# Kernel tuning notes

Measured on AMD Instinct MI355X. Metric: run time of the kernel, lower is better.

Reference implementation:

```python
import jax, jax.numpy as jnp
import numpy as np

# Mamba-2 dims (from wrapper: d_model=hidden_size=2048, d_state=64, d_conv=4, expand=2, headdim=64)
D_MODEL = 2048
EXPAND = 2
HEADDIM = 64
D_STATE = 64
D_CONV = 4
D_INNER = EXPAND * D_MODEL            # 4096
NHEADS = D_INNER // HEADDIM           # 64
NGROUPS = 1                           # mamba_ssm default
CONV_DIM = D_INNER + 2 * NGROUPS * D_STATE          # 4224
D_IN_PROJ = 2 * D_INNER + 2 * NGROUPS * D_STATE + NHEADS  # 8384
BATCH = 1
SEQLEN = 1024
RMS_EPS = 1e-5


def setup_inputs() -> dict:
    key = jax.random.key(0)
    ks = jax.random.split(key, 8)
    x = jax.random.normal(ks[0], (BATCH, SEQLEN, D_MODEL), jnp.float32)
    W_in = jax.random.normal(ks[1], (D_IN_PROJ, D_MODEL), jnp.float32) * 0.02
    conv_w = jax.random.normal(ks[2], (CONV_DIM, D_CONV), jnp.float32) * 0.2
    conv_b = jnp.zeros((CONV_DIM,), jnp.float32)
    # dt_bias so that softplus(dt_raw + dt_bias) lands in a realistic dt range ~[1e-3, 5e-2]
    dt_bias = jax.random.uniform(ks[3], (NHEADS,), jnp.float32, -6.0, -3.0)
    # A = -exp(A_log), A_log init like mamba_ssm: A ~ Uniform(1, 16)
    A_log = jnp.log(1.0 + 15.0 * jax.random.uniform(ks[4], (NHEADS,), jnp.float32))
    D = jnp.ones((NHEADS,), jnp.float32)
    norm_w = jnp.ones((D_INNER,), jnp.float32)
    W_out = jax.random.normal(ks[5], (D_MODEL, D_INNER), jnp.float32) * 0.02
    return {"x": x, "W_in": W_in, "conv_w": conv_w, "conv_b": conv_b,
            "dt_bias": dt_bias, "A_log": A_log, "D": D, "norm_w": norm_w, "W_out": W_out}


def reference(x, W_in, conv_w, conv_b, dt_bias, A_log, D, norm_w, W_out):
    B, T, _ = x.shape
    # input projection -> [z | xBC | dt]
    zxbcdt = jnp.einsum('btd,pd->btp', x, W_in)
    z = zxbcdt[..., :D_INNER]                                  # [B,T,D_INNER] gate
    xBC = zxbcdt[..., D_INNER:D_INNER + CONV_DIM]              # [B,T,CONV_DIM]
    dt = jax.nn.softplus(zxbcdt[..., D_INNER + CONV_DIM:] + dt_bias)  # [B,T,H]
    # causal depthwise conv1d (kernel D_CONV) + SiLU
    xp = jnp.pad(xBC, ((0, 0), (D_CONV - 1, 0), (0, 0)))
    conv = conv_b + sum(xp[:, k:k + T, :] * conv_w[:, k] for k in range(D_CONV))
    xBC = jax.nn.silu(conv)
    xh = xBC[..., :D_INNER].reshape(B, T, NHEADS, HEADDIM)     # [B,T,H,P]
    Bm = xBC[..., D_INNER:D_INNER + D_STATE]                   # [B,T,N] (ngroups=1)
    Cm = xBC[..., D_INNER + D_STATE:]                          # [B,T,N]
    A = -jnp.exp(A_log)                                        # [H], negative
    dA = jnp.exp(dt * A)                                       # [B,T,H] decay per step

    def step(h, inp):
        # h: [B,H,P,N]
        dA_t, dt_t, B_t, x_t, C_t = inp
        h = h * dA_t[:, :, None, None] + jnp.einsum('bh,bn,bhp->bhpn', dt_t, B_t, x_t)
        y_t = jnp.einsum('bhpn,bn->bhp', h, C_t)
        return h, y_t

    h0 = jnp.zeros((B, NHEADS, HEADDIM, D_STATE), x.dtype)
    xs = (dA.transpose(1, 0, 2), dt.transpose(1, 0, 2), Bm.transpose(1, 0, 2),
          xh.transpose(1, 0, 2, 3), Cm.transpose(1, 0, 2))
    _, ys = jax.lax.scan(step, h0, xs)                         # ys: [T,B,H,P]
    y = ys.transpose(1, 0, 2, 3) + D[None, None, :, None] * xh  # skip term D*x
    y = y.reshape(B, T, D_INNER)
    # gated RMSNorm (norm_before_gate=False): norm(y * silu(z)) * weight
    y = y * jax.nn.silu(z)
    y = y * jax.lax.rsqrt(jnp.mean(y * y, axis=-1, keepdims=True) + RMS_EPS) * norm_w
    return jnp.einsum('bti,di->btd', y, W_out)
```

## Files before the change

### kernel.cpp

```cpp
#include <hip/hip_runtime.h>
#include <hip/hip_bf16.h>
#include <stdint.h>

#define SEQLEN   1024
#define DMODEL   2048
#define DINNER   4096
#define NHEADS   64
#define HEADDIM  64
#define DSTATE   64
#define CONVDIM  4224
#define DINPROJ  8384
#define RMS_EPS  1e-5f
#define CPAD     68

typedef __attribute__((ext_vector_type(8))) __bf16 bf16x8;
typedef __attribute__((ext_vector_type(4))) float f32x4;

__device__ __forceinline__ ushort f2bf(float f) {
    uint32_t u = __float_as_uint(f);
    u += 0x7FFFu + ((u >> 16) & 1u);
    return (ushort)(u >> 16);
}

__device__ __forceinline__ float silu(float a) { return a / (1.f + __expf(-a)); }

__device__ __forceinline__ void gload_lds16(const void* g, void* l) {
    __builtin_amdgcn_global_load_lds(
        (const __attribute__((address_space(1))) void*)g,
        (__attribute__((address_space(3))) void*)l, 16, 0, 0);
}

__global__ __launch_bounds__(256) void cvt3_kernel(
    const float* __restrict__ a, ushort* __restrict__ oa, int na4,
    const float* __restrict__ b, ushort* __restrict__ ob, int nb4,
    const float* __restrict__ c, ushort* __restrict__ oc, int nc4)
{
    int i = blockIdx.x * 256 + threadIdx.x;
    const float* src; ushort* dst;
    if (i < na4) { src = a; dst = oa; }
    else if (i < na4 + nb4) { i -= na4; src = b; dst = ob; }
    else { i -= na4 + nb4; if (i >= nc4) return; src = c; dst = oc; }
    float4 v = ((const float4*)src)[i];
    ushort4 o;
    o.x = f2bf(v.x); o.y = f2bf(v.y); o.z = f2bf(v.z); o.w = f2bf(v.w);
    ((ushort4*)dst)[i] = o;
}

__global__ __launch_bounds__(256, 2) void gemm4_bf16_nt(
    const __bf16* __restrict__ A, const __bf16* __restrict__ B,
    float* __restrict__ C, int M, int N, int K,
    int ntx, int nty, int nk, int ksteps, int swz)
{
    __shared__ __align__(16) __bf16 As[2][128 * 64];
    __shared__ __align__(16) __bf16 Bs[2][128 * 64];
    const int tid  = threadIdx.x;
    const int lane = tid & 63;
    const int wave = tid >> 6;
    const int wr = wave >> 1, wc = wave & 1;
    int id = blockIdx.x;
    if (swz) { int q = (ntx * nty * nk) >> 3; id = (id & 7) * q + (id >> 3); }
    const int kz  = id / (ntx * nty);
    const int rem = id % (ntx * nty);
    const int tx = rem / nty, ty = rem % nty;
    const int row0 = ty * 128, col0 = tx * 128;
    const int lr = lane & 15, lq = lane >> 4;
    const int rA = lane >> 3, jl = lane & 7;
    const int k0 = kz * ksteps * 64;

    const __bf16* srcA[4];
    const __bf16* srcB[4];
    int dstAB[4];
    #pragma unroll
    for (int e = 0; e < 4; ++e) {
        int r0 = (wave * 4 + e) * 8;
        int r  = r0 + rA;
        int jg = jl ^ (r & 7);
        srcA[e] = A + (size_t)(row0 + r) * K + k0 + jg * 8;
        int gb = col0 + r; if (gb > N - 1) gb = N - 1;
        srcB[e] = B + (size_t)gb * K + k0 + jg * 8;
        dstAB[e] = r0 * 64;
    }

    f32x4 acc[4][4] = {};
    const int nt = ksteps;

#define STAGE(BUF)                                                            \
    _Pragma("unroll")                                                         \
    for (int e = 0; e < 4; ++e) {                                             \
        gload_lds16(srcA[e], &As[BUF][dstAB[e]]);                             \
        gload_lds16(srcB[e], &Bs[BUF][dstAB[e]]);                             \
        srcA[e] += 64; srcB[e] += 64;                                         \
    }

#define COMPUTE(BUF)                                                          \
    _Pragma("unroll")                                                         \
    for (int kk = 0; kk < 2; ++kk) {                                          \
        const int kg = kk * 4 + lq;                                           \
        bf16x8 af[4], bfr[4];                                                 \
        _Pragma("unroll")                                                     \
        for (int m = 0; m < 4; ++m) {                                         \
            int r = wr * 64 + m * 16 + lr;                                    \
            af[m] = *(const bf16x8*)(&As[BUF][r * 64 + ((kg ^ (r & 7)) * 8)]);\
        }                                                                     \
        _Pragma("unroll")                                                     \
        for (int n = 0; n < 4; ++n) {                                         \
            int r = wc * 64 + n * 16 + lr;                                    \
            bfr[n] = *(const bf16x8*)(&Bs[BUF][r * 64 + ((kg ^ (r & 7)) * 8)]);\
        }                                                                     \
        __builtin_amdgcn_s_setprio(1);                                        \
        _Pragma("unroll")                                                     \
        for (int m = 0; m < 4; ++m)                                           \
            _Pragma("unroll")                                                 \
            for (int n = 0; n < 4; ++n)                                       \
                acc[m][n] = __builtin_amdgcn_mfma_f32_16x16x32_bf16(af[m], bfr[n], acc[m][n], 0, 0, 0); \
        __builtin_amdgcn_s_setprio(0);                                        \
    }

    STAGE(0);
    asm volatile("s_waitcnt vmcnt(0)" ::: "memory");
    __builtin_amdgcn_s_barrier();
    asm volatile("" ::: "memory");

    for (int t = 0; t < nt; t += 2) {
        STAGE(1);
        COMPUTE(0);
        asm volatile("s_waitcnt vmcnt(0)" ::: "memory");
        __builtin_amdgcn_s_barrier();
        asm volatile("" ::: "memory");
        if (t + 2 < nt) { STAGE(0); }
        COMPUTE(1);
        asm volatile("s_waitcnt vmcnt(0)" ::: "memory");
        __builtin_amdgcn_s_barrier();
        asm volatile("" ::: "memory");
    }
#undef STAGE
#undef COMPUTE

    float* Co = C + (size_t)kz * M * N;
    #pragma unroll
    for (int m = 0; m < 4; ++m)
        #pragma unroll
        for (int n = 0; n < 4; ++n) {
            int col = col0 + wc * 64 + n * 16 + lr;
            if (col < N) {
                #pragma unroll
                for (int j = 0; j < 4; ++j) {
                    int row = row0 + wr * 64 + m * 16 + lq * 4 + j;
                    Co[(size_t)row * N + col] = acc[m][n][j];
                }
            }
        }
}

__global__ __launch_bounds__(256) void reduce4_scale_kernel(
    const float* __restrict__ p, const float* __restrict__ ssbuf,
    float* __restrict__ out, int n4)
{
    int i = blockIdx.x * 256 + threadIdx.x;
    if (i < n4) {
        int t = i >> 9;
        float sc = rsqrtf(ssbuf[t] * (1.f / DINNER) + RMS_EPS);
        float4 a = ((const float4*)p)[i];
        float4 b = ((const float4*)p)[i + n4];
        float4 c = ((const float4*)p)[i + 2 * (size_t)n4];
        float4 d = ((const float4*)p)[i + 3 * (size_t)n4];
        float4 o = {(a.x + b.x + c.x + d.x) * sc, (a.y + b.y + c.y + d.y) * sc,
                    (a.z + b.z + c.z + d.z) * sc, (a.w + b.w + c.w + d.w) * sc};
        ((float4*)out)[i] = o;
    }
}

__global__ __launch_bounds__(256) void chunk_intra_kernel(
    const float* __restrict__ zx, const float* __restrict__ conv_w,
    const float* __restrict__ conv_b, const float* __restrict__ dt_bias,
    const float* __restrict__ A_log,
    float* __restrict__ x_scan, float* __restrict__ Cb,
    float* __restrict__ yintra, float* __restrict__ Tc, float* __restrict__ Ssum)
{
    const int head  = blockIdx.x >> 4;
    const int chunk = blockIdx.x & 15;
    const int t0 = chunk * 64;
    const int tid = threadIdx.x;
    const int ty = tid >> 4, tx = tid & 15;
    const int lane = tid & 63, wv = tid >> 6;

    __shared__ __align__(16) float Xs [64][CPAD];
    __shared__ __align__(16) float BsT[64][CPAD];
    __shared__ __align__(16) float CsT[64][CPAD];
    __shared__ __align__(16) float GsT[64][CPAD];
    __shared__ float Sc[64], dts[64], ws[64];

    {
        const int c0 = head * 64 + tx * 4;
        float4 w0 = *(const float4*)&conv_w[(c0 + 0) * 4];
        float4 w1 = *(const float4*)&conv_w[(c0 + 1) * 4];
        float4 w2 = *(const float4*)&conv_w[(c0 + 2) * 4];
        float4 w3 = *(const float4*)&conv_w[(c0 + 3) * 4];
        float4 bv = *(const float4*)&conv_b[c0];
        #pragma unroll
        for (int pass = 0; pass < 4; ++pass) {
            int s = pass * 16 + ty;
            int gt = t0 + s;
            float4 r0 = {0,0,0,0}, r1 = {0,0,0,0}, r2 = {0,0,0,0}, r3;
            const float* base = zx + (size_t)gt * DINPROJ + DINNER + c0;
            if (gt >= 3) r0 = *(const float4*)(base - 3 * DINPROJ);
            if (gt >= 2) r1 = *(const float4*)(base - 2 * DINPROJ);
            if (gt >= 1) r2 = *(const float4*)(base - 1 * DINPROJ);
            r3 = *(const float4*)base;
            float4 o;
            o.x = silu(bv.x + r0.x*w0.x + r1.x*w0.y + r2.x*w0.z + r3.x*w0.w);
            o.y = silu(bv.y + r0.y*w1.x + r1.y*w1.y + r2.y*w1.z + r3.y*w1.w);
            o.z = silu(bv.z + r0.z*w2.x + r1.z*w2.y + r2.z*w2.z + r3.z*w2.w);
            o.w = silu(bv.w + r0.w*w3.x + r1.w*w3.y + r2.w*w3.z + r3.w*w3.w);
            *(float4*)&Xs[s][tx * 4] = o;
            *(float4*)&x_scan[(size_t)gt * DINNER + head * 64 + tx * 4] = o;
        }
    }

    #pragma unroll
    for (int k = 0; k < 4; ++k) {
        int n0 = wv * 16 + k * 4;
        int gt = t0 + lane;
        {
            float4 w0 = *(const float4*)&conv_w[(4096 + n0 + 0) * 4];
            float4 w1 = *(const float4*)&conv_w[(4096 + n0 + 1) * 4];
            float4 w2 = *(const float4*)&conv_w[(4096 + n0 + 2) * 4];
            float4 w3 = *(const float4*)&conv_w[(4096 + n0 + 3) * 4];
            float4 bv = *(const float4*)&conv_b[4096 + n0];
            float4 r0 = {0,0,0,0}, r1 = {0,0,0,0}, r2 = {0,0,0,0}, r3;
            const float* base = zx + (size_t)gt * DINPROJ + 8192 + n0;
            if (gt >= 3) r0 = *(const float4*)(base - 3 * DINPROJ);
            if (gt >= 2) r1 = *(const float4*)(base - 2 * DINPROJ);
            if (gt >= 1) r2 = *(const float4*)(base - 1 * DINPROJ);
            r3 = *(const float4*)base;
            BsT[n0+0][lane] = silu(bv.x + r0.x*w0.x + r1.x*w0.y + r2.x*w0.z + r3.x*w0.w);
            BsT[n0+1][lane] = silu(bv.y + r0.y*w1.x + r1.y*w1.y + r2.y*w1.z + r3.y*w1.w);
            BsT[n0+2][lane] = silu(bv.z + r0.z*w2.x + r1.z*w2.y + r2.z*w2.z + r3.z*w2.w);
            BsT[n0+3][lane] = silu(bv.w + r0.w*w3.x + r1.w*w3.y + r2.w*w3.z + r3.w*w3.w);
        }
        {
            float4 w0 = *(const float4*)&conv_w[(4160 + n0 + 0) * 4];
            float4 w1 = *(const float4*)&conv_w[(4160 + n0 + 1) * 4];
            float4 w2 = *(const float4*)&conv_w[(4160 + n0 + 2) * 4];
            float4 w3 = *(const float4*)&conv_w[(4160 + n0 + 3) * 4];
            float4 bv = *(const float4*)&conv_b[4160 + n0];
            float4 r0 = {0,0,0,0}, r1 = {0,0,0,0}, r2 = {0,0,0,0}, r3;
            const float* base = zx + (size_t)gt * DINPROJ + 8256 + n0;
            if (gt >= 3) r0 = *(const float4*)(base - 3 * DINPROJ);
            if (gt >= 2) r1 = *(const float4*)(base - 2 * DINPROJ);
            if (gt >= 1) r2 = *(const float4*)(base - 1 * DINPROJ);
            r3 = *(const float4*)base;
            float4 cv;
            cv.x = silu(bv.x + r0.x*w0.x + r1.x*w0.y + r2.x*w0.z + r3.x*w0.w);
            cv.y = silu(bv.y + r0.y*w1.x + r1.y*w1.y + r2.y*w1.z + r3.y*w1.w);
            cv.z = silu(bv.z + r0.z*w2.x + r1.z*w2.y + r2.z*w2.z + r3.z*w2.w);
            cv.w = silu(bv.w + r0.w*w3.x + r1.w*w3.y + r2.w*w3.z + r3.w*w3.w);
            CsT[n0+0][lane] = cv.x; CsT[n0+1][lane] = cv.y;
            CsT[n0+2][lane] = cv.z; CsT[n0+3][lane] = cv.w;
            if (head == 0) *(float4*)&Cb[(size_t)gt * 64 + n0] = cv;
        }
    }

    if (wv == 1) {
        float raw = zx[(size_t)(t0 + lane) * DINPROJ + 8320 + head] + dt_bias[head];
        float dt  = (raw > 20.f) ? raw : log1pf(__expf(raw));
        dts[lane] = dt;
        float v = dt * (-__expf(A_log[head]));
        #pragma unroll
        for (int off = 1; off < 64; off <<= 1) {
            float u = __shfl_up(v, off, 64);
            if (lane >= off) v += u;
        }
        Sc[lane] = v;
        Ssum[(t0 + lane) * 64 + head] = v;
    }
    __syncthreads();
    if (tid < 64) ws[tid] = dts[tid] * __expf(Sc[63] - Sc[tid]);

    float gacc[4][4] = {};
    for (int n = 0; n < 64; ++n) {
        float4 ci = *(const float4*)&CsT[n][ty * 4];
        float4 bs = *(const float4*)&BsT[n][tx * 4];
        gacc[0][0] += ci.x*bs.x; gacc[0][1] += ci.x*bs.y; gacc[0][2] += ci.x*bs.z; gacc[0][3] += ci.x*bs.w;
        gacc[1][0] += ci.y*bs.x; gacc[1][1] += ci.y*bs.y; gacc[1][2] += ci.y*bs.z; gacc[1][3] += ci.y*bs.w;
        gacc[2][0] += ci.z*bs.x; gacc[2][1] += ci.z*bs.y; gacc[2][2] += ci.z*bs.z; gacc[2][3] += ci.z*bs.w;
        gacc[3][0] += ci.w*bs.x; gacc[3][1] += ci.w*bs.y; gacc[3][2] += ci.w*bs.z; gacc[3][3] += ci.w*bs.w;
    }
    {
        float Si[4];
        #pragma unroll
        for (int di = 0; di < 4; ++di) Si[di] = Sc[ty * 4 + di];
        #pragma unroll
        for (int ds = 0; ds < 4; ++ds) {
            int s = tx * 4 + ds;
            float dw = dts[s], Ss_ = Sc[s];
            float4 g;
            g.x = (s <= ty*4+0) ? gacc[0][ds] * dw * __expf(Si[0] - Ss_) : 0.f;
            g.y = (s <= ty*4+1) ? gacc[1][ds] * dw * __expf(Si[1] - Ss_) : 0.f;
            g.z = (s <= ty*4+2) ? gacc[2][ds] * dw * __expf(Si[2] - Ss_) : 0.f;
            g.w = (s <= ty*4+3) ? gacc[3][ds] * dw * __expf(Si[3] - Ss_) : 0.f;
            *(float4*)&GsT[s][ty * 4] = g;
        }
    }
    __syncthreads();
    {
        int nn = wv * 16 + (lane >> 2);
        int s0 = (lane & 3) * 16;
        #pragma unroll
        for (int k = 0; k < 4; ++k) {
            float4 b = *(const float4*)&BsT[nn][s0 + k * 4];
            CsT[s0 + k*4 + 0][nn] = b.x;
            CsT[s0 + k*4 + 1][nn] = b.y;
            CsT[s0 + k*4 + 2][nn] = b.z;
            CsT[s0 + k*4 + 3][nn] = b.w;
        }
    }
    __syncthreads();

    float yacc[4][4] = {};
    float tacc[4][4] = {};
    for (int s = 0; s < 64; ++s) {
        float4 g  = *(const float4*)&GsT[s][ty * 4];
        float4 xp = *(const float4*)&Xs[s][tx * 4];
        float4 xq = *(const float4*)&Xs[s][ty * 4];
        float4 bn = *(const float4*)&CsT[s][tx * 4];
        float w = ws[s];
        yacc[0][0] += g.x*xp.x; yacc[0][1] += g.x*xp.y; yacc[0][2] += g.x*xp.z; yacc[0][3] += g.x*xp.w;
        yacc[1][0] += g.y*xp.x; yacc[1][1] += g.y*xp.y; yacc[1][2] += g.y*xp.z; yacc[1][3] += g.y*xp.w;
        yacc[2][0] += g.z*xp.x; yacc[2][1] += g.z*xp.y; yacc[2][2] += g.z*xp.z; yacc[2][3] += g.z*xp.w;
        yacc[3][0] += g.w*xp.x; yacc[3][1] += g.w*xp.y; yacc[3][2] += g.w*xp.z; yacc[3][3] += g.w*xp.w;
        float wx0 = xq.x * w, wx1 = xq.y * w, wx2 = xq.z * w, wx3 = xq.w * w;
        tacc[0][0] += wx0*bn.x; tacc[0][1] += wx0*bn.y; tacc[0][2] += wx0*bn.z; tacc[0][3] += wx0*bn.w;
        tacc[1][0] += wx1*bn.x; tacc[1][1] += wx1*bn.y; tacc[1][2] += wx1*bn.z; tacc[1][3] += wx1*bn.w;
        tacc[2][0] += wx2*bn.x; tacc[2][1] += wx2*bn.y; tacc[2][2] += wx2*bn.z; tacc[2][3] += wx2*bn.w;
        tacc[3][0] += wx3*bn.x; tacc[3][1] += wx3*bn.y; tacc[3][2] += wx3*bn.z; tacc[3][3] += wx3*bn.w;
    }
    #pragma unroll
    for (int di = 0; di < 4; ++di) {
        float4 yv = {yacc[di][0], yacc[di][1], yacc[di][2], yacc[di][3]};
        *(float4*)&yintra[(size_t)(t0 + ty*4 + di) * DINNER + head * 64 + tx * 4] = yv;
    }
    float* tcb = Tc + (size_t)(head * 16 + chunk) * 4096;
    #pragma unroll
    for (int dq = 0; dq < 4; ++dq) {
        float4 tv = {tacc[dq][0], tacc[dq][1], tacc[dq][2], tacc[dq][3]};
        *(float4*)&tcb[(ty*4 + dq) * 64 + tx * 4] = tv;
    }
}

__global__ __launch_bounds__(256) void chunk_state_kernel(
    float* __restrict__ Tc, const float* __restrict__ Ssum)
{
    const int head = blockIdx.x;
    const int tid = threadIdx.x;
    float h[16] = {};
    float* base = Tc + (size_t)head * 16 * 4096 + tid * 16;
    for (int c = 0; c < 16; ++c) {
        float Q = __expf(Ssum[(c * 64 + 63) * 64 + head]);
        float4* p = (float4*)(base + (size_t)c * 4096);
        #pragma unroll
        for (int v = 0; v < 4; ++v) {
            float4 t = p[v];
            float4 hold = {h[v*4], h[v*4+1], h[v*4+2], h[v*4+3]};
            h[v*4+0] = h[v*4+0] * Q + t.x;
            h[v*4+1] = h[v*4+1] * Q + t.y;
            h[v*4+2] = h[v*4+2] * Q + t.z;
            h[v*4+3] = h[v*4+3] * Q + t.w;
            p[v] = hold;
        }
    }
}

__global__ __launch_bounds__(256) void inter_combine_kernel(
    const float* __restrict__ Hpre, const float* __restrict__ Cb,
    const float* __restrict__ Ssum, const float* __restrict__ yintra,
    const float* __restrict__ x_scan, const float* __restrict__ zx,
    const float* __restrict__ Dv, const float* __restrict__ norm_w,
    ushort* __restrict__ ybf, float* __restrict__ ssbuf)
{
    const int head  = blockIdx.x >> 4;
    const int chunk = blockIdx.x & 15;
    const int t0 = chunk * 64;
    const int tid = threadIdx.x;
    const int ty = tid >> 4, tx = tid & 15;
    const int lane = tid & 63, wv = tid >> 6;

    __shared__ __align__(16) float HsT[64][CPAD];
    __shared__ __align__(16) float CsT[64][CPAD];
    __shared__ float Se[64];

    const float* hb = Hpre + (size_t)(head * 16 + chunk) * 4096;
    #pragma unroll
    for (int k = 0; k < 4; ++k) {
        int n0 = wv * 16 + k * 4;
        float4 h = *(const float4*)&hb[lane * 64 + n0];
        float4 c = *(const float4*)&Cb[(t0 + lane) * 64 + n0];
        HsT[n0][lane] = h.x; HsT[n0+1][lane] = h.y; HsT[n0+2][lane] = h.z; HsT[n0+3][lane] = h.w;
        CsT[n0][lane] = c.x; CsT[n0+1][lane] = c.y; CsT[n0+2][lane] = c.z; CsT[n0+3][lane] = c.w;
    }
    if (tid < 64) Se[tid] = __expf(Ssum[(t0 + tid) * 64 + head]);
    __syncthreads();

    float acc[4][4] = {};
    for (int n = 0; n < 64; ++n) {
        float4 ci = *(const float4*)&CsT[n][ty * 4];
        float4 hp = *(const float4*)&HsT[n][tx * 4];
        acc[0][0] += ci.x*hp.x; acc[0][1] += ci.x*hp.y; acc[0][2] += ci.x*hp.z; acc[0][3] += ci.x*hp.w;
        acc[1][0] += ci.y*hp.x; acc[1][1] += ci.y*hp.y; acc[1][2] += ci.y*hp.z; acc[1][3] += ci.y*hp.w;
        acc[2][0] += ci.z*hp.x; acc[2][1] += ci.z*hp.y; acc[2][2] += ci.z*hp.z; acc[2][3] += ci.z*hp.w;
        acc[3][0] += ci.w*hp.x; acc[3][1] += ci.w*hp.y; acc[3][2] += ci.w*hp.z; acc[3][3] += ci.w*hp.w;
    }

    const float Dh = Dv[head];
    const int col = head * 64 + tx * 4;
    float4 nw = *(const float4*)&norm_w[col];
    float ssp[4];
    #pragma unroll
    for (int di = 0; di < 4; ++di) {
        int t = t0 + ty * 4 + di;
        float se = Se[ty * 4 + di];
        float4 yi = *(const float4*)&yintra[(size_t)t * DINNER + col];
        float4 xh = *(const float4*)&x_scan[(size_t)t * DINNER + col];
        float4 zv = *(const float4*)&zx[(size_t)t * DINPROJ + col];
        float4 y;
        y.x = (acc[di][0] * se + yi.x + Dh * xh.x) * silu(zv.x);
        y.y = (acc[di][1] * se + yi.y + Dh * xh.y) * silu(zv.y);
        y.z = (acc[di][2] * se + yi.z + Dh * xh.z) * silu(zv.z);
        y.w = (acc[di][3] * se + yi.w + Dh * xh.w) * silu(zv.w);
        ssp[di] = y.x*y.x + y.y*y.y + y.z*y.z + y.w*y.w;
        ushort4 o;
        o.x = f2bf(y.x * nw.x); o.y = f2bf(y.y * nw.y);
        o.z = f2bf(y.z * nw.z); o.w = f2bf(y.w * nw.w);
        *(ushort4*)&ybf[(size_t)t * DINNER + col] = o;
    }
    #pragma unroll
    for (int di = 0; di < 4; ++di) {
        float s = ssp[di];
        s += __shfl_xor(s, 1, 64);
        s += __shfl_xor(s, 2, 64);
        s += __shfl_xor(s, 4, 64);
        s += __shfl_xor(s, 8, 64);
        if (tx == 0) atomicAdd(&ssbuf[t0 + ty * 4 + di], s);
    }
}

extern "C" void kernel_launch(void* const* d_in, const int* in_sizes, int n_in,
                              void* d_out, int out_size, void* d_ws, size_t ws_size,
                              hipStream_t stream)
{
    const float* x       = (const float*)d_in[0];
    const float* W_in    = (const float*)d_in[1];
    const float* conv_w  = (const float*)d_in[2];
    const float* conv_b  = (const float*)d_in[3];
    const float* dt_bias = (const float*)d_in[4];
    const float* A_log   = (const float*)d_in[5];
    const float* Dv      = (const float*)d_in[6];
    const float* norm_w  = (const float*)d_in[7];
    const float* W_out   = (const float*)d_in[8];
    float* out = (float*)d_out;

    char* ws = (char*)d_ws;
    const size_t OFF_WIN  = 0;
    const size_t OFF_WOUT = 34340864;
    const size_t OFF_XBF  = OFF_WOUT + 16777216;
    const size_t OFF_ZX   = OFF_XBF + 4194304;
    const size_t OFF_XSC  = OFF_ZX + 34340864;
    const size_t OFF_CB   = OFF_XSC + 16777216;
    const size_t OFF_SSB  = OFF_CB + 262144;
    const size_t OFF_YBF  = OFF_SSB + 4096;
    const size_t OFF_TC   = OFF_YBF + 8388608;
    const size_t OFF_SS   = OFF_TC + 16777216;

    ushort* WinBf  = (ushort*)(ws + OFF_WIN);
    ushort* WoutBf = (ushort*)(ws + OFF_WOUT);
    ushort* xBf    = (ushort*)(ws + OFF_XBF);
    float*  zxb    = (float*)(ws + OFF_ZX);
    float*  xsc    = (float*)(ws + OFF_XSC);
    float*  Cb     = (float*)(ws + OFF_CB);
    float*  ssbuf  = (float*)(ws + OFF_SSB);
    ushort* ybf    = (ushort*)(ws + OFF_YBF);
    float*  Tc     = (float*)(ws + OFF_TC);
    float*  Ssum   = (float*)(ws + OFF_SS);
    float*  yintra = (float*)(ws + OFF_WIN);
    float*  part   = (float*)(ws + OFF_WIN + 16777216);

    const int nW4 = DINPROJ * DMODEL / 4;
    const int nO4 = DMODEL * DINNER / 4;
    const int nX4 = SEQLEN * DMODEL / 4;
    const int nAll = nW4 + nO4 + nX4;
    cvt3_kernel<<<(nAll + 255) / 256, 256, 0, stream>>>(
        W_in, WinBf, nW4, W_out, WoutBf, nO4, x, xBf, nX4);

    hipMemsetAsync(ssbuf, 0, SEQLEN * sizeof(float), stream);

    gemm4_bf16_nt<<<528, 256, 0, stream>>>(
        (const __bf16*)xBf, (const __bf16*)WinBf, zxb,
        SEQLEN, DINPROJ, DMODEL, 66, 8, 1, DMODEL / 64, 1);

    chunk_intra_kernel<<<1024, 256, 0, stream>>>(
        zxb, conv_w, conv_b, dt_bias, A_log, xsc, Cb, yintra, Tc, Ssum);

    chunk_state_kernel<<<64, 256, 0, stream>>>(Tc, Ssum);

    inter_combine_kernel<<<1024, 256, 0, stream>>>(
        Tc, Cb, Ssum, yintra, xsc, zxb, Dv, norm_w, ybf, ssbuf);

    gemm4_bf16_nt<<<512, 256, 0, stream>>>(
        (const __bf16*)ybf, (const __bf16*)WoutBf, part,
        SEQLEN, DMODEL, DINNER, 16, 8, 4, DINNER / 64 / 4, 1);

    reduce4_scale_kernel<<<(SEQLEN * DMODEL / 4 + 255) / 256, 256, 0, stream>>>(
        part, ssbuf, out, SEQLEN * DMODEL / 4);
}
```

Measured before the change: 219.2 us.

## Use 8-wave GEMM with 4-stage LDS pipeline and halve out-proj split-K

The bf16 GEMM now runs 512-thread blocks of 8 waves, each wave computing a 64x32 sub-tile. It replaces double buffering with a 4-buffer LDS ring that keeps three stages in flight, using graded vmcnt waits and a single barrier per k-step. The output projection uses split-K of 2 instead of 4, so the reduction kernel sums two partials and moves less partial-sum traffic. The costs are 128KB of LDS per block, which allows one block per CU, and half as many blocks for the output GEMM.

```diff
diff --git a/kernel.cpp b/kernel.cpp
--- a/kernel.cpp
+++ b/kernel.cpp
@@ -46,17 +46,17 @@
     ((ushort4*)dst)[i] = o;
 }
 
-__global__ __launch_bounds__(256, 2) void gemm4_bf16_nt(
+__global__ __launch_bounds__(512, 1) void gemm8_bf16_nt(
     const __bf16* __restrict__ A, const __bf16* __restrict__ B,
     float* __restrict__ C, int M, int N, int K,
     int ntx, int nty, int nk, int ksteps, int swz)
 {
-    __shared__ __align__(16) __bf16 As[2][128 * 64];
-    __shared__ __align__(16) __bf16 Bs[2][128 * 64];
+    __shared__ __align__(16) __bf16 As[4][128 * 64];
+    __shared__ __align__(16) __bf16 Bs[4][128 * 64];
     const int tid  = threadIdx.x;
     const int lane = tid & 63;
     const int wave = tid >> 6;
-    const int wr = wave >> 1, wc = wave & 1;
+    const int wr = wave >> 2, wc = wave & 3;
     int id = blockIdx.x;
     if (swz) { int q = (ntx * nty * nk) >> 3; id = (id & 7) * q + (id >> 3); }
     const int kz  = id / (ntx * nty);
@@ -67,28 +67,29 @@
     const int rA = lane >> 3, jl = lane & 7;
     const int k0 = kz * ksteps * 64;
 
-    const __bf16* srcA[4];
-    const __bf16* srcB[4];
-    int dstAB[4];
-    #pragma unroll
-    for (int e = 0; e < 4; ++e) {
-        int r0 = (wave * 4 + e) * 8;
+    const __bf16* srcA[2];
+    const __bf16* srcB[2];
+    int dstA[2], dstB[2];
+    #pragma unroll
+    for (int e = 0; e < 2; ++e) {
+        int r0 = wave * 16 + e * 8;
         int r  = r0 + rA;
         int jg = jl ^ (r & 7);
         srcA[e] = A + (size_t)(row0 + r) * K + k0 + jg * 8;
+        dstA[e] = r0 * 64;
         int gb = col0 + r; if (gb > N - 1) gb = N - 1;
         srcB[e] = B + (size_t)gb * K + k0 + jg * 8;
-        dstAB[e] = r0 * 64;
-    }
-
-    f32x4 acc[4][4] = {};
+        dstB[e] = r0 * 64;
+    }
+
+    f32x4 acc[4][2] = {};
     const int nt = ksteps;
 
 #define STAGE(BUF)                                                            \
     _Pragma("unroll")                                                         \
-    for (int e = 0; e < 4; ++e) {                                             \
-        gload_lds16(srcA[e], &As[BUF][dstAB[e]]);                             \
-        gload_lds16(srcB[e], &Bs[BUF][dstAB[e]]);                             \
+    for (int e = 0; e < 2; ++e) {                                             \
+        gload_lds16(srcA[e], &As[BUF][dstA[e]]);                              \
+        gload_lds16(srcB[e], &Bs[BUF][dstB[e]]);                              \
         srcA[e] += 64; srcB[e] += 64;                                         \
     }
 
@@ -96,42 +97,38 @@
     _Pragma("unroll")                                                         \
     for (int kk = 0; kk < 2; ++kk) {                                          \
         const int kg = kk * 4 + lq;                                           \
-        bf16x8 af[4], bfr[4];                                                 \
+        bf16x8 af[4], bfr[2];                                                 \
         _Pragma("unroll")                                                     \
         for (int m = 0; m < 4; ++m) {                                         \
             int r = wr * 64 + m * 16 + lr;                                    \
             af[m] = *(const bf16x8*)(&As[BUF][r * 64 + ((kg ^ (r & 7)) * 8)]);\
         }                                                                     \
         _Pragma("unroll")                                                     \
-        for (int n = 0; n < 4; ++n) {                                         \
-            int r = wc * 64 + n * 16 + lr;                                    \
+        for (int n = 0; n < 2; ++n) {                                         \
+            int r = wc * 32 + n * 16 + lr;                                    \
             bfr[n] = *(const bf16x8*)(&Bs[BUF][r * 64 + ((kg ^ (r & 7)) * 8)]);\
         }                                                                     \
         __builtin_amdgcn_s_setprio(1);                                        \
         _Pragma("unroll")                                                     \
         for (int m = 0; m < 4; ++m)                                           \
             _Pragma("unroll")                                                 \
-            for (int n = 0; n < 4; ++n)                                       \
+            for (int n = 0; n < 2; ++n)                                       \
                 acc[m][n] = __builtin_amdgcn_mfma_f32_16x16x32_bf16(af[m], bfr[n], acc[m][n], 0, 0, 0); \
         __builtin_amdgcn_s_setprio(0);                                        \
     }
 
-    STAGE(0);
-    asm volatile("s_waitcnt vmcnt(0)" ::: "memory");
-    __builtin_amdgcn_s_barrier();
-    asm volatile("" ::: "memory");
-
-    for (int t = 0; t < nt; t += 2) {
-        STAGE(1);
-        COMPUTE(0);
-        asm volatile("s_waitcnt vmcnt(0)" ::: "memory");
+    STAGE(0); STAGE(1); STAGE(2);
+
+    for (int t = 0; t < nt; ++t) {
+        const int remk = nt - 1 - t;
+        if (remk >= 2)      asm volatile("s_waitcnt vmcnt(8)" ::: "memory");
+        else if (remk == 1) asm volatile("s_waitcnt vmcnt(4)" ::: "memory");
+        else                asm volatile("s_waitcnt vmcnt(0)" ::: "memory");
         __builtin_amdgcn_s_barrier();
         asm volatile("" ::: "memory");
-        if (t + 2 < nt) { STAGE(0); }
-        COMPUTE(1);
-        asm volatile("s_waitcnt vmcnt(0)" ::: "memory");
-        __builtin_amdgcn_s_barrier();
-        asm volatile("" ::: "memory");
+        const int b = t & 3;
+        COMPUTE(b);
+        if (t + 3 < nt) { STAGE((t + 3) & 3); }
     }
 #undef STAGE
 #undef COMPUTE
@@ -140,8 +137,8 @@
     #pragma unroll
     for (int m = 0; m < 4; ++m)
         #pragma unroll
-        for (int n = 0; n < 4; ++n) {
-            int col = col0 + wc * 64 + n * 16 + lr;
+        for (int n = 0; n < 2; ++n) {
+            int col = col0 + wc * 32 + n * 16 + lr;
             if (col < N) {
                 #pragma unroll
                 for (int j = 0; j < 4; ++j) {
@@ -152,7 +149,7 @@
         }
 }
 
-__global__ __launch_bounds__(256) void reduce4_scale_kernel(
+__global__ __launch_bounds__(256) void reduce2_scale_kernel(
     const float* __restrict__ p, const float* __restrict__ ssbuf,
     float* __restrict__ out, int n4)
 {
@@ -162,10 +159,8 @@
         float sc = rsqrtf(ssbuf[t] * (1.f / DINNER) + RMS_EPS);
         float4 a = ((const float4*)p)[i];
         float4 b = ((const float4*)p)[i + n4];
-        float4 c = ((const float4*)p)[i + 2 * (size_t)n4];
-        float4 d = ((const float4*)p)[i + 3 * (size_t)n4];
-        float4 o = {(a.x + b.x + c.x + d.x) * sc, (a.y + b.y + c.y + d.y) * sc,
-                    (a.z + b.z + c.z + d.z) * sc, (a.w + b.w + c.w + d.w) * sc};
+        float4 o = {(a.x + b.x) * sc, (a.y + b.y) * sc,
+                    (a.z + b.z) * sc, (a.w + b.w) * sc};
         ((float4*)out)[i] = o;
     }
 }
@@ -493,7 +488,7 @@
 
     hipMemsetAsync(ssbuf, 0, SEQLEN * sizeof(float), stream);
 
-    gemm4_bf16_nt<<<528, 256, 0, stream>>>(
+    gemm8_bf16_nt<<<528, 512, 0, stream>>>(
         (const __bf16*)xBf, (const __bf16*)WinBf, zxb,
         SEQLEN, DINPROJ, DMODEL, 66, 8, 1, DMODEL / 64, 1);
 
@@ -505,10 +500,10 @@
     inter_combine_kernel<<<1024, 256, 0, stream>>>(
         Tc, Cb, Ssum, yintra, xsc, zxb, Dv, norm_w, ybf, ssbuf);
 
-    gemm4_bf16_nt<<<512, 256, 0, stream>>>(
+    gemm8_bf16_nt<<<256, 512, 0, stream>>>(
         (const __bf16*)ybf, (const __bf16*)WoutBf, part,
-        SEQLEN, DMODEL, DINNER, 16, 8, 4, DINNER / 64 / 4, 1);
-
-    reduce4_scale_kernel<<<(SEQLEN * DMODEL / 4 + 255) / 256, 256, 0, stream>>>(
+        SEQLEN, DMODEL, DINNER, 16, 8, 2, DINNER / 64 / 2, 1);
+
+    reduce2_scale_kernel<<<(SEQLEN * DMODEL / 4 + 255) / 256, 256, 0, stream>>>(
         part, ssbuf, out, SEQLEN * DMODEL / 4);
 }
```

After: 213.6 us. -2.5%, faster.
